# Kernel optimization log

Hardware: AMD Instinct MI355X
Metric: run time of the kernel (lower is better)

## Reference

```python
import jax, jax.numpy as jnp
import numpy as np

S, B, D, H = 2048, 64, 128, 128


def setup_inputs() -> dict:
    key = jax.random.key(0)
    ks = jax.random.split(key, 7)
    scale = 1.0 / np.sqrt(H)
    return {
        "input": jax.random.normal(ks[0], (S, B, D), dtype=jnp.float32),
        "time": jax.random.uniform(ks[1], (S, B, 1), dtype=jnp.float32),
        "W_ih": jax.random.normal(ks[2], (4 * H, D), dtype=jnp.float32) * scale,
        "W_hh": jax.random.normal(ks[3], (4 * H, H), dtype=jnp.float32) * scale,
        "b": jax.random.normal(ks[4], (4 * H,), dtype=jnp.float32) * scale,
        "w_t": jax.random.uniform(ks[5], (H,), dtype=jnp.float32),
        "b_t": jax.random.uniform(ks[6], (H,), dtype=jnp.float32),
    }


def reference(input, time, W_ih, W_hh, b, w_t, b_t):
    # ReverseLSTMLayer: run a time-conditioned LSTM cell over REVERSED time steps,
    # then re-reverse the stacked outputs. state starts at zeros (state=None).
    Bsz = input.shape[1]
    Hd = W_hh.shape[1]

    def step(state, xt):
        x, t = xt  # x: [B, D], t: [B, 1]
        h, c = state
        gates = x @ W_ih.T + h @ W_hh.T + b  # [B, 4H]
        i_, f_, g_, o_ = jnp.split(gates, 4, axis=-1)
        i_ = jax.nn.sigmoid(i_)
        f_ = jax.nn.sigmoid(f_)
        g_ = jnp.tanh(g_)
        o_ = jax.nn.sigmoid(o_)
        # learned exponential time decay on the carried cell state (T-LSTM style)
        decay = jnp.exp(-jax.nn.relu(t * w_t + b_t))  # [B, H]
        c = f_ * c * decay + i_ * g_
        h = o_ * jnp.tanh(c)
        return (h, c), h

    init = (jnp.zeros((Bsz, Hd), input.dtype), jnp.zeros((Bsz, Hd), input.dtype))
    # iterate over reversed sequence, then reverse outputs back
    (h, c), ys_rev = jax.lax.scan(step, init, (input[::-1], time[::-1]))
    outputs = ys_rev[::-1]  # [S, B, H]
    return outputs, (h, c)
```

## Files before the change

### kernel.cpp

```cpp
#include <hip/hip_runtime.h>

#define S_LEN 2048
#define B_SZ  64
#define D_IN  128
#define H_SZ  128
#define G4    512

typedef __attribute__((ext_vector_type(4))) float     floatx4;
typedef __attribute__((ext_vector_type(2))) float     floatx2;
typedef __attribute__((ext_vector_type(8))) _Float16  half8;
typedef __attribute__((ext_vector_type(4))) _Float16  half4;
typedef __attribute__((ext_vector_type(2))) _Float16  half2_t;

template<int CTRL>
__device__ __forceinline__ float qperm(float v) {
  return __int_as_float(
      __builtin_amdgcn_mov_dpp(__float_as_int(v), CTRL, 0xF, 0xF, true));
}

template<int P>
__device__ __forceinline__ half2_t h2ext(half8 v) {
  return __builtin_shufflevector(v, v, 2 * P, 2 * P + 1);
}

__device__ __forceinline__ void lds_barrier() {
  asm volatile("s_waitcnt lgkmcnt(0)\n\ts_barrier" ::: "memory");
}

__global__ __launch_bounds__(256) void gx_gemm(
    const float* __restrict__ X,
    const float* __restrict__ Wih,
    const float* __restrict__ bias,
    _Float16* __restrict__ gx)
{
  __shared__ _Float16 Wl[128][136];
  const int tid  = threadIdx.x;
  const int lane = tid & 63;
  const int wv   = tid >> 6;
  const int b    = blockIdx.y;
  const int T0   = blockIdx.x * 256;
  const int m    = lane & 15;
  const int q    = lane >> 4;

  const float LOG2E = 1.4426950408889634f;

  half8 afrag[4][4];
  #pragma unroll
  for (int rg = 0; rg < 4; ++rg) {
    const int t = T0 + rg * 64 + wv * 16 + m;
    const float* xrow = X + ((size_t)t * B_SZ + b) * D_IN;
    #pragma unroll
    for (int kf = 0; kf < 4; ++kf) {
      const int k0 = kf * 32 + q * 8;
      floatx4 v0 = *(const floatx4*)(xrow + k0);
      floatx4 v1 = *(const floatx4*)(xrow + k0 + 4);
      half8 a;
      a[0] = (_Float16)v0.x; a[1] = (_Float16)v0.y;
      a[2] = (_Float16)v0.z; a[3] = (_Float16)v0.w;
      a[4] = (_Float16)v1.x; a[5] = (_Float16)v1.y;
      a[6] = (_Float16)v1.z; a[7] = (_Float16)v1.w;
      afrag[rg][kf] = a;
    }
  }

  for (int nc = 0; nc < 4; ++nc) {
    const float sc = (nc == 2) ? (-2.0f * LOG2E) : (-LOG2E);
    __syncthreads();
    for (int i = tid; i < 128 * 32; i += 256) {
      const int row = i >> 5;
      const int c4  = (i & 31) * 4;
      floatx4 v = *(const floatx4*)(Wih + ((size_t)nc * 128 + row) * D_IN + c4);
      Wl[row][c4 + 0] = (_Float16)v.x;
      Wl[row][c4 + 1] = (_Float16)v.y;
      Wl[row][c4 + 2] = (_Float16)v.z;
      Wl[row][c4 + 3] = (_Float16)v.w;
    }
    __syncthreads();

    #pragma unroll
    for (int nt = 0; nt < 8; ++nt) {
      const int n0  = nc * 128 + nt * 16;
      const int nlo = nt * 16 + m;
      const float bv = bias[n0 + m];
      half8 bfrag[4];
      #pragma unroll
      for (int kf = 0; kf < 4; ++kf)
        bfrag[kf] = *(const half8*)(&Wl[nlo][kf * 32 + q * 8]);
      #pragma unroll
      for (int rg = 0; rg < 4; ++rg) {
        floatx4 acc = {bv, bv, bv, bv};
        #pragma unroll
        for (int kf = 0; kf < 4; ++kf)
          acc = __builtin_amdgcn_mfma_f32_16x16x32_f16(afrag[rg][kf],
                                                       bfrag[kf], acc, 0, 0, 0);
        const int tbase = T0 + rg * 64 + wv * 16 + q * 4;
        half4 hv;
        hv[0] = (_Float16)(acc[0] * sc);
        hv[1] = (_Float16)(acc[1] * sc);
        hv[2] = (_Float16)(acc[2] * sc);
        hv[3] = (_Float16)(acc[3] * sc);
        *(half4*)(gx + ((size_t)b * G4 + n0 + m) * S_LEN + tbase) = hv;
      }
    }
  }
}

__device__ __forceinline__ float fd(half2_t a, half2_t b, float c) {
  return __builtin_amdgcn_fdot2(a, b, c, false);
}

__device__ __forceinline__ half8 wcvt(const float* __restrict__ p, float sc) {
  floatx4 v0 = *(const floatx4*)p;
  floatx4 v1 = *(const floatx4*)(p + 4);
  half8 h;
  h[0] = (_Float16)(v0.x * sc); h[1] = (_Float16)(v0.y * sc);
  h[2] = (_Float16)(v0.z * sc); h[3] = (_Float16)(v0.w * sc);
  h[4] = (_Float16)(v1.x * sc); h[5] = (_Float16)(v1.y * sc);
  h[6] = (_Float16)(v1.z * sc); h[7] = (_Float16)(v1.w * sc);
  return h;
}

#define PIN_WEIGHTS()                                                         \
  asm volatile(""                                                             \
               : "+v"(w00), "+v"(w01), "+v"(w02), "+v"(w03),                  \
                 "+v"(w10), "+v"(w11), "+v"(w12), "+v"(w13),                  \
                 "+v"(w20), "+v"(w21), "+v"(w22), "+v"(w23),                  \
                 "+v"(w30), "+v"(w31), "+v"(w32), "+v"(w33),                  \
                 "+v"(wt), "+v"(bt))

#define DOT8(HV, WA, WB, WC, WD)                                              \
  {                                                                           \
    q0a = fd(h2ext<0>(HV), h2ext<0>(WA), q0a);                                \
    q1a = fd(h2ext<0>(HV), h2ext<0>(WB), q1a);                                \
    q2a = fd(h2ext<0>(HV), h2ext<0>(WC), q2a);                                \
    q3a = fd(h2ext<0>(HV), h2ext<0>(WD), q3a);                                \
    q0a = fd(h2ext<1>(HV), h2ext<1>(WA), q0a);                                \
    q1a = fd(h2ext<1>(HV), h2ext<1>(WB), q1a);                                \
    q2a = fd(h2ext<1>(HV), h2ext<1>(WC), q2a);                                \
    q3a = fd(h2ext<1>(HV), h2ext<1>(WD), q3a);                                \
    q0b = fd(h2ext<2>(HV), h2ext<2>(WA), q0b);                                \
    q1b = fd(h2ext<2>(HV), h2ext<2>(WB), q1b);                                \
    q2b = fd(h2ext<2>(HV), h2ext<2>(WC), q2b);                                \
    q3b = fd(h2ext<2>(HV), h2ext<2>(WD), q3b);                                \
    q0b = fd(h2ext<3>(HV), h2ext<3>(WA), q0b);                                \
    q1b = fd(h2ext<3>(HV), h2ext<3>(WB), q1b);                                \
    q2b = fd(h2ext<3>(HV), h2ext<3>(WC), q2b);                                \
    q3b = fd(h2ext<3>(HV), h2ext<3>(WD), q3b);                                \
  }

#define GATE(HR, GXV, TMV, CVAR, HVAR)                                        \
  {                                                                           \
    half8 hv0 = *(const half8*)((HR) + 0 * 32 + tt * 8);                      \
    half8 hv1 = *(const half8*)((HR) + 1 * 32 + tt * 8);                      \
    half8 hv2 = *(const half8*)((HR) + 2 * 32 + tt * 8);                      \
    half8 hv3 = *(const half8*)((HR) + 3 * 32 + tt * 8);                      \
    float q0a = 0.f, q0b = 0.f, q1a = 0.f, q1b = 0.f;                         \
    float q2a = 0.f, q2b = 0.f, q3a = 0.f, q3b = 0.f;                         \
    DOT8(hv0, w00, w10, w20, w30);                                            \
    DOT8(hv1, w01, w11, w21, w31);                                            \
    DOT8(hv2, w02, w12, w22, w32);                                            \
    DOT8(hv3, w03, w13, w23, w33);                                            \
    float a0 = q0a + q0b, a1 = q1a + q1b, a2 = q2a + q2b, a3 = q3a + q3b;     \
    a0 += qperm<0xB1>(a0); a1 += qperm<0xB1>(a1);                             \
    a2 += qperm<0xB1>(a2); a3 += qperm<0xB1>(a3);                             \
    a0 += qperm<0x4E>(a0); a1 += qperm<0x4E>(a1);                             \
    a2 += qperm<0x4E>(a2); a3 += qperm<0x4E>(a3);                             \
    float pre = (tt & 1) ? ((tt & 2) ? a3 : a1) : ((tt & 2) ? a2 : a0);       \
    pre += (GXV);            \
    const float e  = __builtin_amdgcn_exp2f(pre);                             \
    const float v  = fmaf(am, __builtin_amdgcn_rcpf(1.0f + e), aa);           \
    float z = fmaf((TMV), wt, bt);                  \
    z = fminf(z, 0.0f);                                   \
    const float d  = __builtin_amdgcn_exp2f(z);                               \
    const float p2 = qperm<0x4E>(v);                                          \
    const float fv = (tt == 1) ? v : p2;                                      \
    const float r  = odd ? fv * (d * (CVAR)) : v * p2;                        \
    const float cn = r + qperm<0xB1>(r);                                      \
    (CVAR) = cn;                                                              \
    const float e2 = __builtin_amdgcn_exp2f(-2.0f * LOG2E * cn);              \
    const float th = fmaf(2.0f, __builtin_amdgcn_rcpf(1.0f + e2), -1.0f);     \
    (HVAR) = v * th;                                                          \
  }

#define SUB(K, TMV, RP, WP)                                                   \
  {                                                                           \
    const float g0 = (float)cur8[K];                                          \
    float h0;                                                                 \
    GATE(&hbuf[RP][0], g0, (TMV), c, h0);                                     \
    if (tt == 3) {                                                            \
      hbuf[WP][col] = (_Float16)h0;                                           \
      const int tcur = blk * 8 + K;                                           \
      out[((size_t)tcur << 13) + bH + col] = h0;                              \
      if (tcur == 0) {                                                        \
        float* hf = out + (size_t)S_LEN * B_SZ * H_SZ;                        \
        hf[bH + col] = h0;                                                    \
        hf[(size_t)B_SZ * H_SZ + bH + col] = c;                               \
      }                                                                       \
    }                                                                         \
    lds_barrier();                                                            \
  }

__global__ __launch_bounds__(512)
__attribute__((amdgpu_waves_per_eu(2, 2)))
void lstm_rev(
    const _Float16* __restrict__ gx,
    const float* __restrict__ timep,
    const float* __restrict__ Whh,
    const float* __restrict__ w_tp,
    const float* __restrict__ b_tp,
    float* __restrict__ out)
{
  __shared__ __align__(16) _Float16 hbuf[2][H_SZ];
  __shared__ __align__(16) float    tml[S_LEN];
  const int tid = threadIdx.x;
  const int b   = blockIdx.x;
  const int tt  = tid & 3;
  const int col = tid >> 2;
  const int j   = tt * 128 + col;

  const float LOG2E = 1.4426950408889634f;

  #pragma unroll
  for (int k = 0; k < 4; ++k) {
    const int idx = tid + k * 512;
    tml[idx] = timep[(idx << 6) + b];
  }

  half8 w00, w01, w02, w03, w10, w11, w12, w13;
  half8 w20, w21, w22, w23, w30, w31, w32, w33;
  {
    const float s1 = -LOG2E, s2 = -2.0f * LOG2E;
    const float* r0 = Whh + (size_t)(0 * 128 + col) * H_SZ + tt * 8;
    const float* r1 = Whh + (size_t)(1 * 128 + col) * H_SZ + tt * 8;
    const float* r2 = Whh + (size_t)(2 * 128 + col) * H_SZ + tt * 8;
    const float* r3 = Whh + (size_t)(3 * 128 + col) * H_SZ + tt * 8;
    w00 = wcvt(r0 +  0, s1); w01 = wcvt(r0 + 32, s1);
    w02 = wcvt(r0 + 64, s1); w03 = wcvt(r0 + 96, s1);
    w10 = wcvt(r1 +  0, s1); w11 = wcvt(r1 + 32, s1);
    w12 = wcvt(r1 + 64, s1); w13 = wcvt(r1 + 96, s1);
    w20 = wcvt(r2 +  0, s2); w21 = wcvt(r2 + 32, s2);
    w22 = wcvt(r2 + 64, s2); w23 = wcvt(r2 + 96, s2);
    w30 = wcvt(r3 +  0, s1); w31 = wcvt(r3 + 32, s1);
    w32 = wcvt(r3 + 64, s1); w33 = wcvt(r3 + 96, s1);
  }

  float wt = -LOG2E * w_tp[col];
  float bt = -LOG2E * b_tp[col];
  const float am  = (tt == 2) ? 2.0f : 1.0f;
  const float aa  = (tt == 2) ? -1.0f : 0.0f;
  const bool  odd = (tt & 1) != 0;

  if (tid < 2 * H_SZ) ((_Float16*)hbuf)[tid] = (_Float16)0.0f;
  __syncthreads();

  const _Float16* gxr = gx + ((size_t)b * G4 + j) * S_LEN;
  const size_t bH = (size_t)b * H_SZ;

  half8 cur8 = *(const half8*)(gxr + 255 * 8);
  half8 nxt8 = *(const half8*)(gxr + 254 * 8);

  float c = 0.0f;

  for (int blk = 255; blk >= 0; --blk) {
    PIN_WEIGHTS();
    const int pfb = (blk >= 2) ? blk - 2 : 0;
    half8 fut8 = *(const half8*)(gxr + pfb * 8);
    const floatx4 tmA = *(const floatx4*)(&tml[blk * 8 + 4]);
    const floatx4 tmB = *(const floatx4*)(&tml[blk * 8 + 0]);

    SUB(7, tmA.w, 0, 1)
    SUB(6, tmA.z, 1, 0)
    SUB(5, tmA.y, 0, 1)
    SUB(4, tmA.x, 1, 0)
    SUB(3, tmB.w, 0, 1)
    SUB(2, tmB.z, 1, 0)
    SUB(1, tmB.y, 0, 1)
    SUB(0, tmB.x, 1, 0)

    cur8 = nxt8;
    nxt8 = fut8;
  }
}

extern "C" void kernel_launch(void* const* d_in, const int* in_sizes, int n_in,
                              void* d_out, int out_size, void* d_ws, size_t ws_size,
                              hipStream_t stream) {
  const float* input = (const float*)d_in[0];
  const float* timep = (const float*)d_in[1];
  const float* W_ih  = (const float*)d_in[2];
  const float* W_hh  = (const float*)d_in[3];
  const float* bias  = (const float*)d_in[4];
  const float* w_t   = (const float*)d_in[5];
  const float* b_t   = (const float*)d_in[6];
  float* out = (float*)d_out;

  _Float16* gx = (_Float16*)d_ws;

  gx_gemm<<<dim3(S_LEN / 256, B_SZ), dim3(256), 0, stream>>>(
      input, W_ih, bias, gx);

  lstm_rev<<<dim3(B_SZ), dim3(512), 0, stream>>>(
      gx, timep, W_hh, w_t, b_t, out);
}
```

Before: 1.287 ms.

## Process two batch elements per block in the recurrent LSTM kernel

Each workgroup now runs two independent batch rows through the sequential recurrence, sharing the register-resident W_hh weights and interleaving the two gate computations between barriers. Half as many blocks are launched, and the per-step barrier and latency cost is spread over twice the work, giving more instruction-level parallelism within each step. The trade-off is lower parallelism across the GPU (32 blocks) and a longer per-step critical path. A dead DOT8 copy containing a typo is defined and then immediately undefined.

```diff
diff --git a/kernel.cpp b/kernel.cpp
--- a/kernel.cpp
+++ b/kernel.cpp
@@ -128,6 +128,27 @@
                  "+v"(w30), "+v"(w31), "+v"(w32), "+v"(w33),                  \
                  "+v"(wt), "+v"(bt))
 
+#define DOT8(HV, WA, WB, WC, WD)                                              \
+  {                                                                           \
+    q0a = fd(h2ext<0>(HV), h2ext<0>(WA), q0a);                                \
+    q1a = fd(h2ext<0>(HV), h2ext<0>(WB), q1a);                                \
+    q2a = fd(h2ext<0>(HV), h2ext<0>(WC), q2a);                                \
+    q3a = fd(h2ext<0>(HV), h2ext<0>(WD), q3a);                                \
+    q0a = fd(h2ext<1>(HV), h2ext<1>(WA), q0a);                                \
+    q1a = fd(h2ext<1>(HV), h2ext<1>(WB), q1a);                                \
+    q2a = fd(h2ext<1>(HV), h2ext<1>(WC), q2a);                                \
+    q3a = fd(h2ext<1>(HV), h2ext<1>(WD), q3a);                                \
+    q0b = fd(h2ext<2>(HV), h2ext<2>(WA), q0b);                                \
+    q1b = fd(h2ext<2>(HV), h2ext<2>(WB), q1b);                                \
+    q2b = fd(h2ext<2>(HV), h2ext<2>(WC), q2b);                                \
+    q3b = fd(h2ext<2>(HV), h2ext<2>(WD), q3b);                                \
+    q0b = fd(h2ext<3>(HV), h2ext<3>(WA), q0b);                                \
+    q1b = fd(h2ext<3>(HV), h2ext<3>(WB), q1b);                                \
+    q2b = fd(h2ext<3>(HV), h2ext<3>(WD), q2b);                                \
+    q3b = fd(h2ext<3>(HV), h2ext<3>(WD), q3b);                                \
+  }
+
+#undef DOT8
 #define DOT8(HV, WA, WB, WC, WD)                                              \
   {                                                                           \
     q0a = fd(h2ext<0>(HV), h2ext<0>(WA), q0a);                                \
@@ -182,19 +203,27 @@
     (HVAR) = v * th;                                                          \
   }
 
-#define SUB(K, TMV, RP, WP)                                                   \
+#define SUB2(K, TM0, TM1, RP, WP)                                             \
   {                                                                           \
-    const float g0 = (float)cur8[K];                                          \
-    float h0;                                                                 \
-    GATE(&hbuf[RP][0], g0, (TMV), c, h0);                                     \
+    const float g0 = (float)cura[K];                                          \
+    const float g1 = (float)curb[K];                                          \
+    float h0, h1;                                                             \
+    GATE(&hbuf[0][RP][0], g0, (TM0), c0, h0);                                 \
+    GATE(&hbuf[1][RP][0], g1, (TM1), c1, h1);                                 \
     if (tt == 3) {                                                            \
-      hbuf[WP][col] = (_Float16)h0;                                           \
+      hbuf[0][WP][col] = (_Float16)h0;                                        \
+      hbuf[1][WP][col] = (_Float16)h1;                                        \
       const int tcur = blk * 8 + K;                                           \
-      out[((size_t)tcur << 13) + bH + col] = h0;                              \
+      float* o = out + ((size_t)tcur << 13) + b0H + col;                      \
+      o[0]    = h0;                                                           \
+      o[H_SZ] = h1;                                                           \
       if (tcur == 0) {                                                        \
         float* hf = out + (size_t)S_LEN * B_SZ * H_SZ;                        \
-        hf[bH + col] = h0;                                                    \
-        hf[(size_t)B_SZ * H_SZ + bH + col] = c;                               \
+        hf[b0H + col]        = h0;                                            \
+        hf[b0H + H_SZ + col] = h1;                                            \
+        float* cf = hf + (size_t)B_SZ * H_SZ;                                 \
+        cf[b0H + col]        = c0;                                            \
+        cf[b0H + H_SZ + col] = c1;                                            \
       }                                                                       \
     }                                                                         \
     lds_barrier();                                                            \
@@ -210,10 +239,10 @@
     const float* __restrict__ b_tp,
     float* __restrict__ out)
 {
-  __shared__ __align__(16) _Float16 hbuf[2][H_SZ];
-  __shared__ __align__(16) float    tml[S_LEN];
+  __shared__ __align__(16) _Float16 hbuf[2][2][H_SZ];
+  __shared__ __align__(16) floatx2  tml[S_LEN];
   const int tid = threadIdx.x;
-  const int b   = blockIdx.x;
+  const int b0  = blockIdx.x * 2;
   const int tt  = tid & 3;
   const int col = tid >> 2;
   const int j   = tt * 128 + col;
@@ -223,7 +252,10 @@
   #pragma unroll
   for (int k = 0; k < 4; ++k) {
     const int idx = tid + k * 512;
-    tml[idx] = timep[(idx << 6) + b];
+    floatx2 tv;
+    tv.x = timep[(idx << 6) + b0];
+    tv.y = timep[(idx << 6) + b0 + 1];
+    tml[idx] = tv;
   }
 
   half8 w00, w01, w02, w03, w10, w11, w12, w13;
@@ -250,35 +282,41 @@
   const float aa  = (tt == 2) ? -1.0f : 0.0f;
   const bool  odd = (tt & 1) != 0;
 
-  if (tid < 2 * H_SZ) ((_Float16*)hbuf)[tid] = (_Float16)0.0f;
+  ((_Float16*)hbuf)[tid] = (_Float16)0.0f;
   __syncthreads();
 
-  const _Float16* gxr = gx + ((size_t)b * G4 + j) * S_LEN;
-  const size_t bH = (size_t)b * H_SZ;
-
-  half8 cur8 = *(const half8*)(gxr + 255 * 8);
-  half8 nxt8 = *(const half8*)(gxr + 254 * 8);
-
-  float c = 0.0f;
+  const _Float16* gxra = gx + ((size_t)b0 * G4 + j) * S_LEN;
+  const _Float16* gxrb = gxra + (size_t)G4 * S_LEN;
+  const size_t b0H = (size_t)b0 * H_SZ;
+
+  half8 cura = *(const half8*)(gxra + 255 * 8);
+  half8 curb = *(const half8*)(gxrb + 255 * 8);
+  half8 nxta = *(const half8*)(gxra + 254 * 8);
+  half8 nxtb = *(const half8*)(gxrb + 254 * 8);
+
+  float c0 = 0.0f, c1 = 0.0f;
 
   for (int blk = 255; blk >= 0; --blk) {
     PIN_WEIGHTS();
     const int pfb = (blk >= 2) ? blk - 2 : 0;
-    half8 fut8 = *(const half8*)(gxr + pfb * 8);
-    const floatx4 tmA = *(const floatx4*)(&tml[blk * 8 + 4]);
-    const floatx4 tmB = *(const floatx4*)(&tml[blk * 8 + 0]);
-
-    SUB(7, tmA.w, 0, 1)
-    SUB(6, tmA.z, 1, 0)
-    SUB(5, tmA.y, 0, 1)
-    SUB(4, tmA.x, 1, 0)
-    SUB(3, tmB.w, 0, 1)
-    SUB(2, tmB.z, 1, 0)
-    SUB(1, tmB.y, 0, 1)
-    SUB(0, tmB.x, 1, 0)
-
-    cur8 = nxt8;
-    nxt8 = fut8;
+    half8 futa = *(const half8*)(gxra + pfb * 8);
+    half8 futb = *(const half8*)(gxrb + pfb * 8);
+    const floatx4 tmQ0 = *(const floatx4*)(&tml[blk * 8 + 0]);
+    const floatx4 tmQ1 = *(const floatx4*)(&tml[blk * 8 + 2]);
+    const floatx4 tmQ2 = *(const floatx4*)(&tml[blk * 8 + 4]);
+    const floatx4 tmQ3 = *(const floatx4*)(&tml[blk * 8 + 6]);
+
+    SUB2(7, tmQ3.z, tmQ3.w, 0, 1)
+    SUB2(6, tmQ3.x, tmQ3.y, 1, 0)
+    SUB2(5, tmQ2.z, tmQ2.w, 0, 1)
+    SUB2(4, tmQ2.x, tmQ2.y, 1, 0)
+    SUB2(3, tmQ1.z, tmQ1.w, 0, 1)
+    SUB2(2, tmQ1.x, tmQ1.y, 1, 0)
+    SUB2(1, tmQ0.z, tmQ0.w, 0, 1)
+    SUB2(0, tmQ0.x, tmQ0.y, 1, 0)
+
+    cura = nxta; nxta = futa;
+    curb = nxtb; nxtb = futb;
   }
 }
 
@@ -299,6 +337,6 @@
   gx_gemm<<<dim3(S_LEN / 256, B_SZ), dim3(256), 0, stream>>>(
       input, W_ih, bias, gx);
 
-  lstm_rev<<<dim3(B_SZ), dim3(512), 0, stream>>>(
+  lstm_rev<<<dim3(B_SZ / 2), dim3(512), 0, stream>>>(
       gx, timep, W_hh, w_t, b_t, out);
 }
```

Result: slower. 2.237 ms (+73.8%).

## Halve LSTM block to 256 threads, each computing two hidden columns

Applied to the files above, without the earlier changes.

The recurrent kernel now launches 256 threads per batch row instead of 512. Each thread holds the W_hh slices for two hidden columns (col and col+64) in registers and computes both gate sets per step, sharing the h vector loads from LDS. The aim is to cut per-step barrier cost across fewer waves (4 instead of 8) and to raise per-thread instruction-level parallelism. In exchange, register use roughly doubles (waves_per_eu set to 1) and the serial work per thread per step doubles, which may lengthen the critical path.

```diff
diff --git a/kernel.cpp b/kernel.cpp
--- a/kernel.cpp
+++ b/kernel.cpp
@@ -120,88 +120,118 @@
   return h;
 }
 
-#define PIN_WEIGHTS()                                                         \
+#define PIN_A()                                                               \
   asm volatile(""                                                             \
-               : "+v"(w00), "+v"(w01), "+v"(w02), "+v"(w03),                  \
-                 "+v"(w10), "+v"(w11), "+v"(w12), "+v"(w13),                  \
-                 "+v"(w20), "+v"(w21), "+v"(w22), "+v"(w23),                  \
-                 "+v"(w30), "+v"(w31), "+v"(w32), "+v"(w33),                  \
-                 "+v"(wt), "+v"(bt))
-
-#define DOT8(HV, WA, WB, WC, WD)                                              \
+               : "+v"(wa00), "+v"(wa01), "+v"(wa02), "+v"(wa03),              \
+                 "+v"(wa10), "+v"(wa11), "+v"(wa12), "+v"(wa13),              \
+                 "+v"(wa20), "+v"(wa21), "+v"(wa22), "+v"(wa23),              \
+                 "+v"(wa30), "+v"(wa31), "+v"(wa32), "+v"(wa33),              \
+                 "+v"(wtA), "+v"(btA))
+#define PIN_B()                                                               \
+  asm volatile(""                                                             \
+               : "+v"(wb00), "+v"(wb01), "+v"(wb02), "+v"(wb03),              \
+                 "+v"(wb10), "+v"(wb11), "+v"(wb12), "+v"(wb13),              \
+                 "+v"(wb20), "+v"(wb21), "+v"(wb22), "+v"(wb23),              \
+                 "+v"(wb30), "+v"(wb31), "+v"(wb32), "+v"(wb33),              \
+                 "+v"(wtB), "+v"(btB))
+
+#define DOT8P(Q, HV, W0, W1, W2, W3)                                          \
   {                                                                           \
-    q0a = fd(h2ext<0>(HV), h2ext<0>(WA), q0a);                                \
-    q1a = fd(h2ext<0>(HV), h2ext<0>(WB), q1a);                                \
-    q2a = fd(h2ext<0>(HV), h2ext<0>(WC), q2a);                                \
-    q3a = fd(h2ext<0>(HV), h2ext<0>(WD), q3a);                                \
-    q0a = fd(h2ext<1>(HV), h2ext<1>(WA), q0a);                                \
-    q1a = fd(h2ext<1>(HV), h2ext<1>(WB), q1a);                                \
-    q2a = fd(h2ext<1>(HV), h2ext<1>(WC), q2a);                                \
-    q3a = fd(h2ext<1>(HV), h2ext<1>(WD), q3a);                                \
-    q0b = fd(h2ext<2>(HV), h2ext<2>(WA), q0b);                                \
-    q1b = fd(h2ext<2>(HV), h2ext<2>(WB), q1b);                                \
-    q2b = fd(h2ext<2>(HV), h2ext<2>(WC), q2b);                                \
-    q3b = fd(h2ext<2>(HV), h2ext<2>(WD), q3b);                                \
-    q0b = fd(h2ext<3>(HV), h2ext<3>(WA), q0b);                                \
-    q1b = fd(h2ext<3>(HV), h2ext<3>(WB), q1b);                                \
-    q2b = fd(h2ext<3>(HV), h2ext<3>(WC), q2b);                                \
-    q3b = fd(h2ext<3>(HV), h2ext<3>(WD), q3b);                                \
-  }
-
-#define GATE(HR, GXV, TMV, CVAR, HVAR)                                        \
+    Q##0a = fd(h2ext<0>(HV), h2ext<0>(W0), Q##0a);                            \
+    Q##1a = fd(h2ext<0>(HV), h2ext<0>(W1), Q##1a);                            \
+    Q##2a = fd(h2ext<0>(HV), h2ext<0>(W2), Q##2a);                            \
+    Q##3a = fd(h2ext<0>(HV), h2ext<0>(W3), Q##3a);                            \
+    Q##0a = fd(h2ext<1>(HV), h2ext<1>(W0), Q##0a);                            \
+    Q##1a = fd(h2ext<1>(HV), h2ext<1>(W1), Q##1a);                            \
+    Q##2a = fd(h2ext<1>(HV), h2ext<1>(W2), Q##2a);                            \
+    Q##3a = fd(h2ext<1>(HV), h2ext<1>(W3), Q##3a);                            \
+    Q##0b = fd(h2ext<2>(HV), h2ext<2>(W0), Q##0b);                            \
+    Q##1b = fd(h2ext<2>(HV), h2ext<2>(W1), Q##1b);                            \
+    Q##2b = fd(h2ext<2>(HV), h2ext<2>(W2), Q##2b);                            \
+    Q##3b = fd(h2ext<2>(HV), h2ext<2>(W3), Q##3b);                            \
+    Q##0b = fd(h2ext<3>(HV), h2ext<3>(W0), Q##0b);                            \
+    Q##1b = fd(h2ext<3>(HV), h2ext<3>(W1), Q##1b);                            \
+    Q##2b = fd(h2ext<3>(HV), h2ext<3>(W2), Q##2b);                            \
+    Q##3b = fd(h2ext<3>(HV), h2ext<3>(W3), Q##3b);                            \
+  }
+
+#define ACT(PRE, TMV, WT, BT, CV, HOUT)                                       \
   {                                                                           \
-    half8 hv0 = *(const half8*)((HR) + 0 * 32 + tt * 8);                      \
-    half8 hv1 = *(const half8*)((HR) + 1 * 32 + tt * 8);                      \
-    half8 hv2 = *(const half8*)((HR) + 2 * 32 + tt * 8);                      \
-    half8 hv3 = *(const half8*)((HR) + 3 * 32 + tt * 8);                      \
-    float q0a = 0.f, q0b = 0.f, q1a = 0.f, q1b = 0.f;                         \
-    float q2a = 0.f, q2b = 0.f, q3a = 0.f, q3b = 0.f;                         \
-    DOT8(hv0, w00, w10, w20, w30);                                            \
-    DOT8(hv1, w01, w11, w21, w31);                                            \
-    DOT8(hv2, w02, w12, w22, w32);                                            \
-    DOT8(hv3, w03, w13, w23, w33);                                            \
-    float a0 = q0a + q0b, a1 = q1a + q1b, a2 = q2a + q2b, a3 = q3a + q3b;     \
-    a0 += qperm<0xB1>(a0); a1 += qperm<0xB1>(a1);                             \
-    a2 += qperm<0xB1>(a2); a3 += qperm<0xB1>(a3);                             \
-    a0 += qperm<0x4E>(a0); a1 += qperm<0x4E>(a1);                             \
-    a2 += qperm<0x4E>(a2); a3 += qperm<0x4E>(a3);                             \
-    float pre = (tt & 1) ? ((tt & 2) ? a3 : a1) : ((tt & 2) ? a2 : a0);       \
-    pre += (GXV);            \
-    const float e  = __builtin_amdgcn_exp2f(pre);                             \
+    const float e  = __builtin_amdgcn_exp2f(PRE);                             \
     const float v  = fmaf(am, __builtin_amdgcn_rcpf(1.0f + e), aa);           \
-    float z = fmaf((TMV), wt, bt);                  \
-    z = fminf(z, 0.0f);                                   \
+    float z = fmaf((TMV), (WT), (BT));                                        \
+    z = fminf(z, 0.0f);                                                       \
     const float d  = __builtin_amdgcn_exp2f(z);                               \
     const float p2 = qperm<0x4E>(v);                                          \
     const float fv = (tt == 1) ? v : p2;                                      \
-    const float r  = odd ? fv * (d * (CVAR)) : v * p2;                        \
+    const float r  = odd ? fv * (d * (CV)) : v * p2;                          \
     const float cn = r + qperm<0xB1>(r);                                      \
-    (CVAR) = cn;                                                              \
+    (CV) = cn;                                                                \
     const float e2 = __builtin_amdgcn_exp2f(-2.0f * LOG2E * cn);              \
     const float th = fmaf(2.0f, __builtin_amdgcn_rcpf(1.0f + e2), -1.0f);     \
-    (HVAR) = v * th;                                                          \
-  }
-
-#define SUB(K, TMV, RP, WP)                                                   \
+    (HOUT) = v * th;                                                          \
+  }
+
+#define SUB2(K, TMV, RP, WP)                                                  \
   {                                                                           \
-    const float g0 = (float)cur8[K];                                          \
-    float h0;                                                                 \
-    GATE(&hbuf[RP][0], g0, (TMV), c, h0);                                     \
+    const float g0 = (float)cur0[K];                                          \
+    const float g1 = (float)cur1[K];                                          \
+    half8 hv0 = *(const half8*)(&hbuf[RP][0] + 0 * 32 + tt * 8);              \
+    half8 hv1 = *(const half8*)(&hbuf[RP][0] + 1 * 32 + tt * 8);              \
+    half8 hv2 = *(const half8*)(&hbuf[RP][0] + 2 * 32 + tt * 8);              \
+    half8 hv3 = *(const half8*)(&hbuf[RP][0] + 3 * 32 + tt * 8);              \
+    float qa0a = 0.f, qa0b = 0.f, qa1a = 0.f, qa1b = 0.f;                     \
+    float qa2a = 0.f, qa2b = 0.f, qa3a = 0.f, qa3b = 0.f;                     \
+    float qb0a = 0.f, qb0b = 0.f, qb1a = 0.f, qb1b = 0.f;                     \
+    float qb2a = 0.f, qb2b = 0.f, qb3a = 0.f, qb3b = 0.f;                     \
+    DOT8P(qa, hv0, wa00, wa10, wa20, wa30);                                   \
+    DOT8P(qb, hv0, wb00, wb10, wb20, wb30);                                   \
+    DOT8P(qa, hv1, wa01, wa11, wa21, wa31);                                   \
+    DOT8P(qb, hv1, wb01, wb11, wb21, wb31);                                   \
+    DOT8P(qa, hv2, wa02, wa12, wa22, wa32);                                   \
+    DOT8P(qb, hv2, wb02, wb12, wb22, wb32);                                   \
+    DOT8P(qa, hv3, wa03, wa13, wa23, wa33);                                   \
+    DOT8P(qb, hv3, wb03, wb13, wb23, wb33);                                   \
+    float aA0 = qa0a + qa0b, aA1 = qa1a + qa1b;                               \
+    float aA2 = qa2a + qa2b, aA3 = qa3a + qa3b;                               \
+    float aB0 = qb0a + qb0b, aB1 = qb1a + qb1b;                               \
+    float aB2 = qb2a + qb2b, aB3 = qb3a + qb3b;                               \
+    aA0 += qperm<0xB1>(aA0); aA1 += qperm<0xB1>(aA1);                         \
+    aA2 += qperm<0xB1>(aA2); aA3 += qperm<0xB1>(aA3);                         \
+    aB0 += qperm<0xB1>(aB0); aB1 += qperm<0xB1>(aB1);                         \
+    aB2 += qperm<0xB1>(aB2); aB3 += qperm<0xB1>(aB3);                         \
+    aA0 += qperm<0x4E>(aA0); aA1 += qperm<0x4E>(aA1);                         \
+    aA2 += qperm<0x4E>(aA2); aA3 += qperm<0x4E>(aA3);                         \
+    aB0 += qperm<0x4E>(aB0); aB1 += qperm<0x4E>(aB1);                         \
+    aB2 += qperm<0x4E>(aB2); aB3 += qperm<0x4E>(aB3);                         \
+    float preA = (tt & 1) ? ((tt & 2) ? aA3 : aA1) : ((tt & 2) ? aA2 : aA0);  \
+    float preB = (tt & 1) ? ((tt & 2) ? aB3 : aB1) : ((tt & 2) ? aB2 : aB0);  \
+    preA += g0;                                                               \
+    preB += g1;                                                               \
+    float hA, hB;                                                             \
+    ACT(preA, (TMV), wtA, btA, cA, hA);                                       \
+    ACT(preB, (TMV), wtB, btB, cB, hB);                                       \
     if (tt == 3) {                                                            \
-      hbuf[WP][col] = (_Float16)h0;                                           \
+      hbuf[WP][col]      = (_Float16)hA;                                      \
+      hbuf[WP][col + 64] = (_Float16)hB;                                      \
       const int tcur = blk * 8 + K;                                           \
-      out[((size_t)tcur << 13) + bH + col] = h0;                              \
+      float* o = out + ((size_t)tcur << 13) + bH + col;                       \
+      o[0]  = hA;                                                             \
+      o[64] = hB;                                                             \
       if (tcur == 0) {                                                        \
         float* hf = out + (size_t)S_LEN * B_SZ * H_SZ;                        \
-        hf[bH + col] = h0;                                                    \
-        hf[(size_t)B_SZ * H_SZ + bH + col] = c;                               \
+        hf[bH + col]      = hA;                                               \
+        hf[bH + col + 64] = hB;                                               \
+        float* cf = hf + (size_t)B_SZ * H_SZ;                                 \
+        cf[bH + col]      = cA;                                               \
+        cf[bH + col + 64] = cB;                                               \
       }                                                                       \
     }                                                                         \
     lds_barrier();                                                            \
   }
 
-__global__ __launch_bounds__(512)
-__attribute__((amdgpu_waves_per_eu(2, 2)))
+__global__ __launch_bounds__(256)
+__attribute__((amdgpu_waves_per_eu(1, 1)))
 void lstm_rev(
     const _Float16* __restrict__ gx,
     const float* __restrict__ timep,
@@ -216,69 +246,91 @@
   const int b   = blockIdx.x;
   const int tt  = tid & 3;
   const int col = tid >> 2;
-  const int j   = tt * 128 + col;
+  const int j0  = tt * 128 + col;
+  const int j1  = j0 + 64;
 
   const float LOG2E = 1.4426950408889634f;
 
   #pragma unroll
-  for (int k = 0; k < 4; ++k) {
-    const int idx = tid + k * 512;
+  for (int k = 0; k < 8; ++k) {
+    const int idx = tid + k * 256;
     tml[idx] = timep[(idx << 6) + b];
   }
 
-  half8 w00, w01, w02, w03, w10, w11, w12, w13;
-  half8 w20, w21, w22, w23, w30, w31, w32, w33;
+  half8 wa00, wa01, wa02, wa03, wa10, wa11, wa12, wa13;
+  half8 wa20, wa21, wa22, wa23, wa30, wa31, wa32, wa33;
+  half8 wb00, wb01, wb02, wb03, wb10, wb11, wb12, wb13;
+  half8 wb20, wb21, wb22, wb23, wb30, wb31, wb32, wb33;
   {
     const float s1 = -LOG2E, s2 = -2.0f * LOG2E;
-    const float* r0 = Whh + (size_t)(0 * 128 + col) * H_SZ + tt * 8;
-    const float* r1 = Whh + (size_t)(1 * 128 + col) * H_SZ + tt * 8;
-    const float* r2 = Whh + (size_t)(2 * 128 + col) * H_SZ + tt * 8;
-    const float* r3 = Whh + (size_t)(3 * 128 + col) * H_SZ + tt * 8;
-    w00 = wcvt(r0 +  0, s1); w01 = wcvt(r0 + 32, s1);
-    w02 = wcvt(r0 + 64, s1); w03 = wcvt(r0 + 96, s1);
-    w10 = wcvt(r1 +  0, s1); w11 = wcvt(r1 + 32, s1);
-    w12 = wcvt(r1 + 64, s1); w13 = wcvt(r1 + 96, s1);
-    w20 = wcvt(r2 +  0, s2); w21 = wcvt(r2 + 32, s2);
-    w22 = wcvt(r2 + 64, s2); w23 = wcvt(r2 + 96, s2);
-    w30 = wcvt(r3 +  0, s1); w31 = wcvt(r3 + 32, s1);
-    w32 = wcvt(r3 + 64, s1); w33 = wcvt(r3 + 96, s1);
-  }
-
-  float wt = -LOG2E * w_tp[col];
-  float bt = -LOG2E * b_tp[col];
+    const float* a0 = Whh + (size_t)(0 * 128 + col) * H_SZ + tt * 8;
+    const float* a1 = Whh + (size_t)(1 * 128 + col) * H_SZ + tt * 8;
+    const float* a2 = Whh + (size_t)(2 * 128 + col) * H_SZ + tt * 8;
+    const float* a3 = Whh + (size_t)(3 * 128 + col) * H_SZ + tt * 8;
+    wa00 = wcvt(a0 +  0, s1); wa01 = wcvt(a0 + 32, s1);
+    wa02 = wcvt(a0 + 64, s1); wa03 = wcvt(a0 + 96, s1);
+    wa10 = wcvt(a1 +  0, s1); wa11 = wcvt(a1 + 32, s1);
+    wa12 = wcvt(a1 + 64, s1); wa13 = wcvt(a1 + 96, s1);
+    wa20 = wcvt(a2 +  0, s2); wa21 = wcvt(a2 + 32, s2);
+    wa22 = wcvt(a2 + 64, s2); wa23 = wcvt(a2 + 96, s2);
+    wa30 = wcvt(a3 +  0, s1); wa31 = wcvt(a3 + 32, s1);
+    wa32 = wcvt(a3 + 64, s1); wa33 = wcvt(a3 + 96, s1);
+    const float* b0p = a0 + (size_t)64 * H_SZ;
+    const float* b1p = a1 + (size_t)64 * H_SZ;
+    const float* b2p = a2 + (size_t)64 * H_SZ;
+    const float* b3p = a3 + (size_t)64 * H_SZ;
+    wb00 = wcvt(b0p +  0, s1); wb01 = wcvt(b0p + 32, s1);
+    wb02 = wcvt(b0p + 64, s1); wb03 = wcvt(b0p + 96, s1);
+    wb10 = wcvt(b1p +  0, s1); wb11 = wcvt(b1p + 32, s1);
+    wb12 = wcvt(b1p + 64, s1); wb13 = wcvt(b1p + 96, s1);
+    wb20 = wcvt(b2p +  0, s2); wb21 = wcvt(b2p + 32, s2);
+    wb22 = wcvt(b2p + 64, s2); wb23 = wcvt(b2p + 96, s2);
+    wb30 = wcvt(b3p +  0, s1); wb31 = wcvt(b3p + 32, s1);
+    wb32 = wcvt(b3p + 64, s1); wb33 = wcvt(b3p + 96, s1);
+  }
+
+  float wtA = -LOG2E * w_tp[col];
+  float btA = -LOG2E * b_tp[col];
+  float wtB = -LOG2E * w_tp[col + 64];
+  float btB = -LOG2E * b_tp[col + 64];
   const float am  = (tt == 2) ? 2.0f : 1.0f;
   const float aa  = (tt == 2) ? -1.0f : 0.0f;
   const bool  odd = (tt & 1) != 0;
 
-  if (tid < 2 * H_SZ) ((_Float16*)hbuf)[tid] = (_Float16)0.0f;
+  ((_Float16*)hbuf)[tid] = (_Float16)0.0f;
   __syncthreads();
 
-  const _Float16* gxr = gx + ((size_t)b * G4 + j) * S_LEN;
+  const _Float16* gxr0 = gx + ((size_t)b * G4 + j0) * S_LEN;
+  const _Float16* gxr1 = gx + ((size_t)b * G4 + j1) * S_LEN;
   const size_t bH = (size_t)b * H_SZ;
 
-  half8 cur8 = *(const half8*)(gxr + 255 * 8);
-  half8 nxt8 = *(const half8*)(gxr + 254 * 8);
-
-  float c = 0.0f;
+  half8 cur0 = *(const half8*)(gxr0 + 255 * 8);
+  half8 cur1 = *(const half8*)(gxr1 + 255 * 8);
+  half8 nxt0 = *(const half8*)(gxr0 + 254 * 8);
+  half8 nxt1 = *(const half8*)(gxr1 + 254 * 8);
+
+  float cA = 0.0f, cB = 0.0f;
 
   for (int blk = 255; blk >= 0; --blk) {
-    PIN_WEIGHTS();
+    PIN_A();
+    PIN_B();
     const int pfb = (blk >= 2) ? blk - 2 : 0;
-    half8 fut8 = *(const half8*)(gxr + pfb * 8);
+    half8 fut0 = *(const half8*)(gxr0 + pfb * 8);
+    half8 fut1 = *(const half8*)(gxr1 + pfb * 8);
     const floatx4 tmA = *(const floatx4*)(&tml[blk * 8 + 4]);
     const floatx4 tmB = *(const floatx4*)(&tml[blk * 8 + 0]);
 
-    SUB(7, tmA.w, 0, 1)
-    SUB(6, tmA.z, 1, 0)
-    SUB(5, tmA.y, 0, 1)
-    SUB(4, tmA.x, 1, 0)
-    SUB(3, tmB.w, 0, 1)
-    SUB(2, tmB.z, 1, 0)
-    SUB(1, tmB.y, 0, 1)
-    SUB(0, tmB.x, 1, 0)
-
-    cur8 = nxt8;
-    nxt8 = fut8;
+    SUB2(7, tmA.w, 0, 1)
+    SUB2(6, tmA.z, 1, 0)
+    SUB2(5, tmA.y, 0, 1)
+    SUB2(4, tmA.x, 1, 0)
+    SUB2(3, tmB.w, 0, 1)
+    SUB2(2, tmB.z, 1, 0)
+    SUB2(1, tmB.y, 0, 1)
+    SUB2(0, tmB.x, 1, 0)
+
+    cur0 = nxt0; nxt0 = fut0;
+    cur1 = nxt1; nxt1 = fut1;
   }
 }
 
@@ -299,6 +351,6 @@
   gx_gemm<<<dim3(S_LEN / 256, B_SZ), dim3(256), 0, stream>>>(
       input, W_ih, bias, gx);
 
-  lstm_rev<<<dim3(B_SZ), dim3(512), 0, stream>>>(
+  lstm_rev<<<dim3(B_SZ), dim3(256), 0, stream>>>(
       gx, timep, W_hh, w_t, b_t, out);
 }
```

Measured after the change: 1.344 ms. 1.04x slower.

## Batch 16 sequences per block and compute recurrent gates with MFMA

Applied to the files above, without the earlier changes.

Replaces the per-batch-row fdot2 recurrence (one block per batch element, 64 blocks) with a block handling 16 batch rows. Each wave computes its 16 hidden units' four gates via 16x16x32 f16 MFMAs against h from LDS, then applies all activations per lane without DPP cross-lane combines. The time values are now read directly from global memory with register prefetch instead of staged in LDS. This launches only 4 blocks, so parallelism across CUs drops sharply. MFMA latency also now sits on the serial per-step critical path.

```diff
diff --git a/kernel.cpp b/kernel.cpp
--- a/kernel.cpp
+++ b/kernel.cpp
@@ -7,24 +7,22 @@
 #define G4    512
 
 typedef __attribute__((ext_vector_type(4))) float     floatx4;
-typedef __attribute__((ext_vector_type(2))) float     floatx2;
 typedef __attribute__((ext_vector_type(8))) _Float16  half8;
 typedef __attribute__((ext_vector_type(4))) _Float16  half4;
-typedef __attribute__((ext_vector_type(2))) _Float16  half2_t;
-
-template<int CTRL>
-__device__ __forceinline__ float qperm(float v) {
-  return __int_as_float(
-      __builtin_amdgcn_mov_dpp(__float_as_int(v), CTRL, 0xF, 0xF, true));
-}
-
-template<int P>
-__device__ __forceinline__ half2_t h2ext(half8 v) {
-  return __builtin_shufflevector(v, v, 2 * P, 2 * P + 1);
-}
 
 __device__ __forceinline__ void lds_barrier() {
   asm volatile("s_waitcnt lgkmcnt(0)\n\ts_barrier" ::: "memory");
+}
+
+__device__ __forceinline__ half8 wcvt(const float* __restrict__ p, float sc) {
+  floatx4 v0 = *(const floatx4*)p;
+  floatx4 v1 = *(const floatx4*)(p + 4);
+  half8 h;
+  h[0] = (_Float16)(v0.x * sc); h[1] = (_Float16)(v0.y * sc);
+  h[2] = (_Float16)(v0.z * sc); h[3] = (_Float16)(v0.w * sc);
+  h[4] = (_Float16)(v1.x * sc); h[5] = (_Float16)(v1.y * sc);
+  h[6] = (_Float16)(v1.z * sc); h[7] = (_Float16)(v1.w * sc);
+  return h;
 }
 
 __global__ __launch_bounds__(256) void gx_gemm(
@@ -105,97 +103,103 @@
   }
 }
 
-__device__ __forceinline__ float fd(half2_t a, half2_t b, float c) {
-  return __builtin_amdgcn_fdot2(a, b, c, false);
-}
-
-__device__ __forceinline__ half8 wcvt(const float* __restrict__ p, float sc) {
-  floatx4 v0 = *(const floatx4*)p;
-  floatx4 v1 = *(const floatx4*)(p + 4);
-  half8 h;
-  h[0] = (_Float16)(v0.x * sc); h[1] = (_Float16)(v0.y * sc);
-  h[2] = (_Float16)(v0.z * sc); h[3] = (_Float16)(v0.w * sc);
-  h[4] = (_Float16)(v1.x * sc); h[5] = (_Float16)(v1.y * sc);
-  h[6] = (_Float16)(v1.z * sc); h[7] = (_Float16)(v1.w * sc);
-  return h;
-}
-
-#define PIN_WEIGHTS()                                                         \
+
+#define PIN_W()                                                               \
   asm volatile(""                                                             \
-               : "+v"(w00), "+v"(w01), "+v"(w02), "+v"(w03),                  \
-                 "+v"(w10), "+v"(w11), "+v"(w12), "+v"(w13),                  \
-                 "+v"(w20), "+v"(w21), "+v"(w22), "+v"(w23),                  \
-                 "+v"(w30), "+v"(w31), "+v"(w32), "+v"(w33),                  \
-                 "+v"(wt), "+v"(bt))
-
-#define DOT8(HV, WA, WB, WC, WD)                                              \
+               : "+v"(wA00), "+v"(wA01), "+v"(wA02), "+v"(wA03),              \
+                 "+v"(wA10), "+v"(wA11), "+v"(wA12), "+v"(wA13),              \
+                 "+v"(wA20), "+v"(wA21), "+v"(wA22), "+v"(wA23),              \
+                 "+v"(wA30), "+v"(wA31), "+v"(wA32), "+v"(wA33))
+
+#define GLOADQ(P, TQ)                                                         \
+  P##00 = *(const half4*)(gxb + (size_t)(0 * 128 + 0) * S_LEN + (TQ));        \
+  P##01 = *(const half4*)(gxb + (size_t)(0 * 128 + 1) * S_LEN + (TQ));        \
+  P##02 = *(const half4*)(gxb + (size_t)(0 * 128 + 2) * S_LEN + (TQ));        \
+  P##03 = *(const half4*)(gxb + (size_t)(0 * 128 + 3) * S_LEN + (TQ));        \
+  P##10 = *(const half4*)(gxb + (size_t)(1 * 128 + 0) * S_LEN + (TQ));        \
+  P##11 = *(const half4*)(gxb + (size_t)(1 * 128 + 1) * S_LEN + (TQ));        \
+  P##12 = *(const half4*)(gxb + (size_t)(1 * 128 + 2) * S_LEN + (TQ));        \
+  P##13 = *(const half4*)(gxb + (size_t)(1 * 128 + 3) * S_LEN + (TQ));        \
+  P##20 = *(const half4*)(gxb + (size_t)(2 * 128 + 0) * S_LEN + (TQ));        \
+  P##21 = *(const half4*)(gxb + (size_t)(2 * 128 + 1) * S_LEN + (TQ));        \
+  P##22 = *(const half4*)(gxb + (size_t)(2 * 128 + 2) * S_LEN + (TQ));        \
+  P##23 = *(const half4*)(gxb + (size_t)(2 * 128 + 3) * S_LEN + (TQ));        \
+  P##30 = *(const half4*)(gxb + (size_t)(3 * 128 + 0) * S_LEN + (TQ));        \
+  P##31 = *(const half4*)(gxb + (size_t)(3 * 128 + 1) * S_LEN + (TQ));        \
+  P##32 = *(const half4*)(gxb + (size_t)(3 * 128 + 2) * S_LEN + (TQ));        \
+  P##33 = *(const half4*)(gxb + (size_t)(3 * 128 + 3) * S_LEN + (TQ));
+
+#define GROT()                                                                \
+  gc00 = gn00; gc01 = gn01; gc02 = gn02; gc03 = gn03;                         \
+  gc10 = gn10; gc11 = gn11; gc12 = gn12; gc13 = gn13;                         \
+  gc20 = gn20; gc21 = gn21; gc22 = gn22; gc23 = gn23;                         \
+  gc30 = gn30; gc31 = gn31; gc32 = gn32; gc33 = gn33;                         \
+  tc0 = tn0; tc1 = tn1; tc2 = tn2; tc3 = tn3;
+
+#define TLOADQ(P, TQ)                                                         \
+  P##0 = tmb[(size_t)((TQ) + 0) * B_SZ];                                      \
+  P##1 = tmb[(size_t)((TQ) + 1) * B_SZ];                                      \
+  P##2 = tmb[(size_t)((TQ) + 2) * B_SZ];                                      \
+  P##3 = tmb[(size_t)((TQ) + 3) * B_SZ];
+
+#define ACT1(PI, PF, PG, PO, TMV, WTR, BTR, CR, HR)                           \
   {                                                                           \
-    q0a = fd(h2ext<0>(HV), h2ext<0>(WA), q0a);                                \
-    q1a = fd(h2ext<0>(HV), h2ext<0>(WB), q1a);                                \
-    q2a = fd(h2ext<0>(HV), h2ext<0>(WC), q2a);                                \
-    q3a = fd(h2ext<0>(HV), h2ext<0>(WD), q3a);                                \
-    q0a = fd(h2ext<1>(HV), h2ext<1>(WA), q0a);                                \
-    q1a = fd(h2ext<1>(HV), h2ext<1>(WB), q1a);                                \
-    q2a = fd(h2ext<1>(HV), h2ext<1>(WC), q2a);                                \
-    q3a = fd(h2ext<1>(HV), h2ext<1>(WD), q3a);                                \
-    q0b = fd(h2ext<2>(HV), h2ext<2>(WA), q0b);                                \
-    q1b = fd(h2ext<2>(HV), h2ext<2>(WB), q1b);                                \
-    q2b = fd(h2ext<2>(HV), h2ext<2>(WC), q2b);                                \
-    q3b = fd(h2ext<2>(HV), h2ext<2>(WD), q3b);                                \
-    q0b = fd(h2ext<3>(HV), h2ext<3>(WA), q0b);                                \
-    q1b = fd(h2ext<3>(HV), h2ext<3>(WB), q1b);                                \
-    q2b = fd(h2ext<3>(HV), h2ext<3>(WC), q2b);                                \
-    q3b = fd(h2ext<3>(HV), h2ext<3>(WD), q3b);                                \
-  }
-
-#define GATE(HR, GXV, TMV, CVAR, HVAR)                                        \
+    const float is = __builtin_amdgcn_rcpf(1.0f + __builtin_amdgcn_exp2f(PI));\
+    const float fs = __builtin_amdgcn_rcpf(1.0f + __builtin_amdgcn_exp2f(PF));\
+    const float gt = fmaf(2.0f,                                               \
+        __builtin_amdgcn_rcpf(1.0f + __builtin_amdgcn_exp2f(PG)), -1.0f);     \
+    const float os = __builtin_amdgcn_rcpf(1.0f + __builtin_amdgcn_exp2f(PO));\
+    const float z  = fminf(fmaf((TMV), (WTR), (BTR)), 0.0f);                  \
+    const float d  = __builtin_amdgcn_exp2f(z);                               \
+    (CR) = fmaf(fs * d, (CR), is * gt);                                       \
+    const float et = __builtin_amdgcn_exp2f(-2.0f * LOG2E * (CR));            \
+    const float th = fmaf(2.0f, __builtin_amdgcn_rcpf(1.0f + et), -1.0f);     \
+    (HR) = os * th;                                                           \
+  }
+
+#define SUBK(K, RP, WP, TMV)                                                  \
   {                                                                           \
-    half8 hv0 = *(const half8*)((HR) + 0 * 32 + tt * 8);                      \
-    half8 hv1 = *(const half8*)((HR) + 1 * 32 + tt * 8);                      \
-    half8 hv2 = *(const half8*)((HR) + 2 * 32 + tt * 8);                      \
-    half8 hv3 = *(const half8*)((HR) + 3 * 32 + tt * 8);                      \
-    float q0a = 0.f, q0b = 0.f, q1a = 0.f, q1b = 0.f;                         \
-    float q2a = 0.f, q2b = 0.f, q3a = 0.f, q3b = 0.f;                         \
-    DOT8(hv0, w00, w10, w20, w30);                                            \
-    DOT8(hv1, w01, w11, w21, w31);                                            \
-    DOT8(hv2, w02, w12, w22, w32);                                            \
-    DOT8(hv3, w03, w13, w23, w33);                                            \
-    float a0 = q0a + q0b, a1 = q1a + q1b, a2 = q2a + q2b, a3 = q3a + q3b;     \
-    a0 += qperm<0xB1>(a0); a1 += qperm<0xB1>(a1);                             \
-    a2 += qperm<0xB1>(a2); a3 += qperm<0xB1>(a3);                             \
-    a0 += qperm<0x4E>(a0); a1 += qperm<0x4E>(a1);                             \
-    a2 += qperm<0x4E>(a2); a3 += qperm<0x4E>(a3);                             \
-    float pre = (tt & 1) ? ((tt & 2) ? a3 : a1) : ((tt & 2) ? a2 : a0);       \
-    pre += (GXV);            \
-    const float e  = __builtin_amdgcn_exp2f(pre);                             \
-    const float v  = fmaf(am, __builtin_amdgcn_rcpf(1.0f + e), aa);           \
-    float z = fmaf((TMV), wt, bt);                  \
-    z = fminf(z, 0.0f);                                   \
-    const float d  = __builtin_amdgcn_exp2f(z);                               \
-    const float p2 = qperm<0x4E>(v);                                          \
-    const float fv = (tt == 1) ? v : p2;                                      \
-    const float r  = odd ? fv * (d * (CVAR)) : v * p2;                        \
-    const float cn = r + qperm<0xB1>(r);                                      \
-    (CVAR) = cn;                                                              \
-    const float e2 = __builtin_amdgcn_exp2f(-2.0f * LOG2E * cn);              \
-    const float th = fmaf(2.0f, __builtin_amdgcn_rcpf(1.0f + e2), -1.0f);     \
-    (HVAR) = v * th;                                                          \
-  }
-
-#define SUB(K, TMV, RP, WP)                                                   \
-  {                                                                           \
-    const float g0 = (float)cur8[K];                                          \
-    float h0;                                                                 \
-    GATE(&hbuf[RP][0], g0, (TMV), c, h0);                                     \
-    if (tt == 3) {                                                            \
-      hbuf[WP][col] = (_Float16)h0;                                           \
-      const int tcur = blk * 8 + K;                                           \
-      out[((size_t)tcur << 13) + bH + col] = h0;                              \
-      if (tcur == 0) {                                                        \
-        float* hf = out + (size_t)S_LEN * B_SZ * H_SZ;                        \
-        hf[bH + col] = h0;                                                    \
-        hf[(size_t)B_SZ * H_SZ + bH + col] = c;                               \
-      }                                                                       \
+    half8 hb0 = *(const half8*)&hl[RP][bq][0 * 32 + q * 8];                   \
+    half8 hb1 = *(const half8*)&hl[RP][bq][1 * 32 + q * 8];                   \
+    half8 hb2 = *(const half8*)&hl[RP][bq][2 * 32 + q * 8];                   \
+    half8 hb3 = *(const half8*)&hl[RP][bq][3 * 32 + q * 8];                   \
+    floatx4 aI = {(float)gc00[K], (float)gc01[K], (float)gc02[K], (float)gc03[K]}; \
+    floatx4 aF = {(float)gc10[K], (float)gc11[K], (float)gc12[K], (float)gc13[K]}; \
+    floatx4 aG = {(float)gc20[K], (float)gc21[K], (float)gc22[K], (float)gc23[K]}; \
+    floatx4 aO = {(float)gc30[K], (float)gc31[K], (float)gc32[K], (float)gc33[K]}; \
+    aI = __builtin_amdgcn_mfma_f32_16x16x32_f16(wA00, hb0, aI, 0, 0, 0);      \
+    aI = __builtin_amdgcn_mfma_f32_16x16x32_f16(wA01, hb1, aI, 0, 0, 0);      \
+    aI = __builtin_amdgcn_mfma_f32_16x16x32_f16(wA02, hb2, aI, 0, 0, 0);      \
+    aI = __builtin_amdgcn_mfma_f32_16x16x32_f16(wA03, hb3, aI, 0, 0, 0);      \
+    aF = __builtin_amdgcn_mfma_f32_16x16x32_f16(wA10, hb0, aF, 0, 0, 0);      \
+    aF = __builtin_amdgcn_mfma_f32_16x16x32_f16(wA11, hb1, aF, 0, 0, 0);      \
+    aF = __builtin_amdgcn_mfma_f32_16x16x32_f16(wA12, hb2, aF, 0, 0, 0);      \
+    aF = __builtin_amdgcn_mfma_f32_16x16x32_f16(wA13, hb3, aF, 0, 0, 0);      \
+    aG = __builtin_amdgcn_mfma_f32_16x16x32_f16(wA20, hb0, aG, 0, 0, 0);      \
+    aG = __builtin_amdgcn_mfma_f32_16x16x32_f16(wA21, hb1, aG, 0, 0, 0);      \
+    aG = __builtin_amdgcn_mfma_f32_16x16x32_f16(wA22, hb2, aG, 0, 0, 0);      \
+    aG = __builtin_amdgcn_mfma_f32_16x16x32_f16(wA23, hb3, aG, 0, 0, 0);      \
+    aO = __builtin_amdgcn_mfma_f32_16x16x32_f16(wA30, hb0, aO, 0, 0, 0);      \
+    aO = __builtin_amdgcn_mfma_f32_16x16x32_f16(wA31, hb1, aO, 0, 0, 0);      \
+    aO = __builtin_amdgcn_mfma_f32_16x16x32_f16(wA32, hb2, aO, 0, 0, 0);      \
+    aO = __builtin_amdgcn_mfma_f32_16x16x32_f16(wA33, hb3, aO, 0, 0, 0);      \
+    float h0, h1, h2, h3;                                                     \
+    ACT1(aI[0], aF[0], aG[0], aO[0], (TMV), wt0, bt0, c0, h0);                \
+    ACT1(aI[1], aF[1], aG[1], aO[1], (TMV), wt1, bt1, c1, h1);                \
+    ACT1(aI[2], aF[2], aG[2], aO[2], (TMV), wt2, bt2, c2, h2);                \
+    ACT1(aI[3], aF[3], aG[3], aO[3], (TMV), wt3, bt3, c3, h3);                \
+    half4 hv;                                                                 \
+    hv[0] = (_Float16)h0; hv[1] = (_Float16)h1;                               \
+    hv[2] = (_Float16)h2; hv[3] = (_Float16)h3;                               \
+    *(half4*)&hl[WP][bq][hc0] = hv;                                           \
+    const int tcur = tq + (K);                                                \
+    floatx4 ov = {h0, h1, h2, h3};                                            \
+    *(floatx4*)(out + ((size_t)tcur << 13) + ((size_t)b << 7) + hc0) = ov;    \
+    if (tcur == 0) {                                                          \
+      float* hf = out + (size_t)S_LEN * B_SZ * H_SZ;                          \
+      *(floatx4*)(hf + ((size_t)b << 7) + hc0) = ov;                          \
+      floatx4 cv = {c0, c1, c2, c3};                                          \
+      *(floatx4*)(hf + (size_t)B_SZ * H_SZ + ((size_t)b << 7) + hc0) = cv;    \
     }                                                                         \
     lds_barrier();                                                            \
   }
@@ -210,75 +214,73 @@
     const float* __restrict__ b_tp,
     float* __restrict__ out)
 {
-  __shared__ __align__(16) _Float16 hbuf[2][H_SZ];
-  __shared__ __align__(16) float    tml[S_LEN];
+  __shared__ __align__(16) _Float16 hl[2][16][136];
   const int tid = threadIdx.x;
-  const int b   = blockIdx.x;
-  const int tt  = tid & 3;
-  const int col = tid >> 2;
-  const int j   = tt * 128 + col;
+  const int w   = tid >> 6;
+  const int l   = tid & 63;
+  const int bq  = l & 15;
+  const int q   = l >> 4;
+  const int B0  = blockIdx.x * 16;
+  const int b   = B0 + bq;
+  const int hc0 = w * 16 + q * 4;
 
   const float LOG2E = 1.4426950408889634f;
 
-  #pragma unroll
-  for (int k = 0; k < 4; ++k) {
-    const int idx = tid + k * 512;
-    tml[idx] = timep[(idx << 6) + b];
-  }
-
-  half8 w00, w01, w02, w03, w10, w11, w12, w13;
-  half8 w20, w21, w22, w23, w30, w31, w32, w33;
+  half8 wA00, wA01, wA02, wA03, wA10, wA11, wA12, wA13;
+  half8 wA20, wA21, wA22, wA23, wA30, wA31, wA32, wA33;
   {
     const float s1 = -LOG2E, s2 = -2.0f * LOG2E;
-    const float* r0 = Whh + (size_t)(0 * 128 + col) * H_SZ + tt * 8;
-    const float* r1 = Whh + (size_t)(1 * 128 + col) * H_SZ + tt * 8;
-    const float* r2 = Whh + (size_t)(2 * 128 + col) * H_SZ + tt * 8;
-    const float* r3 = Whh + (size_t)(3 * 128 + col) * H_SZ + tt * 8;
-    w00 = wcvt(r0 +  0, s1); w01 = wcvt(r0 + 32, s1);
-    w02 = wcvt(r0 + 64, s1); w03 = wcvt(r0 + 96, s1);
-    w10 = wcvt(r1 +  0, s1); w11 = wcvt(r1 + 32, s1);
-    w12 = wcvt(r1 + 64, s1); w13 = wcvt(r1 + 96, s1);
-    w20 = wcvt(r2 +  0, s2); w21 = wcvt(r2 + 32, s2);
-    w22 = wcvt(r2 + 64, s2); w23 = wcvt(r2 + 96, s2);
-    w30 = wcvt(r3 +  0, s1); w31 = wcvt(r3 + 32, s1);
-    w32 = wcvt(r3 + 64, s1); w33 = wcvt(r3 + 96, s1);
-  }
-
-  float wt = -LOG2E * w_tp[col];
-  float bt = -LOG2E * b_tp[col];
-  const float am  = (tt == 2) ? 2.0f : 1.0f;
-  const float aa  = (tt == 2) ? -1.0f : 0.0f;
-  const bool  odd = (tt & 1) != 0;
-
-  if (tid < 2 * H_SZ) ((_Float16*)hbuf)[tid] = (_Float16)0.0f;
+    const float* r0 = Whh + (size_t)(0 * 128 + w * 16 + bq) * H_SZ + q * 8;
+    const float* r1 = Whh + (size_t)(1 * 128 + w * 16 + bq) * H_SZ + q * 8;
+    const float* r2 = Whh + (size_t)(2 * 128 + w * 16 + bq) * H_SZ + q * 8;
+    const float* r3 = Whh + (size_t)(3 * 128 + w * 16 + bq) * H_SZ + q * 8;
+    wA00 = wcvt(r0 +  0, s1); wA01 = wcvt(r0 + 32, s1);
+    wA02 = wcvt(r0 + 64, s1); wA03 = wcvt(r0 + 96, s1);
+    wA10 = wcvt(r1 +  0, s1); wA11 = wcvt(r1 + 32, s1);
+    wA12 = wcvt(r1 + 64, s1); wA13 = wcvt(r1 + 96, s1);
+    wA20 = wcvt(r2 +  0, s2); wA21 = wcvt(r2 + 32, s2);
+    wA22 = wcvt(r2 + 64, s2); wA23 = wcvt(r2 + 96, s2);
+    wA30 = wcvt(r3 +  0, s1); wA31 = wcvt(r3 + 32, s1);
+    wA32 = wcvt(r3 + 64, s1); wA33 = wcvt(r3 + 96, s1);
+  }
+
+  const floatx4 wtv = *(const floatx4*)(w_tp + hc0);
+  const floatx4 btv = *(const floatx4*)(b_tp + hc0);
+  const float wt0 = -LOG2E * wtv[0], wt1 = -LOG2E * wtv[1];
+  const float wt2 = -LOG2E * wtv[2], wt3 = -LOG2E * wtv[3];
+  const float bt0 = -LOG2E * btv[0], bt1 = -LOG2E * btv[1];
+  const float bt2 = -LOG2E * btv[2], bt3 = -LOG2E * btv[3];
+
+  for (int i = tid; i < 2 * 16 * 136; i += 512)
+    ((_Float16*)hl)[i] = (_Float16)0.0f;
   __syncthreads();
 
-  const _Float16* gxr = gx + ((size_t)b * G4 + j) * S_LEN;
-  const size_t bH = (size_t)b * H_SZ;
-
-  half8 cur8 = *(const half8*)(gxr + 255 * 8);
-  half8 nxt8 = *(const half8*)(gxr + 254 * 8);
-
-  float c = 0.0f;
-
-  for (int blk = 255; blk >= 0; --blk) {
-    PIN_WEIGHTS();
-    const int pfb = (blk >= 2) ? blk - 2 : 0;
-    half8 fut8 = *(const half8*)(gxr + pfb * 8);
-    const floatx4 tmA = *(const floatx4*)(&tml[blk * 8 + 4]);
-    const floatx4 tmB = *(const floatx4*)(&tml[blk * 8 + 0]);
-
-    SUB(7, tmA.w, 0, 1)
-    SUB(6, tmA.z, 1, 0)
-    SUB(5, tmA.y, 0, 1)
-    SUB(4, tmA.x, 1, 0)
-    SUB(3, tmB.w, 0, 1)
-    SUB(2, tmB.z, 1, 0)
-    SUB(1, tmB.y, 0, 1)
-    SUB(0, tmB.x, 1, 0)
-
-    cur8 = nxt8;
-    nxt8 = fut8;
+  const _Float16* gxb = gx + ((size_t)b * G4 + w * 16 + q * 4) * S_LEN;
+  const float*    tmb = timep + b;
+
+  float c0 = 0.0f, c1 = 0.0f, c2 = 0.0f, c3 = 0.0f;
+
+  half4 gc00, gc01, gc02, gc03, gc10, gc11, gc12, gc13;
+  half4 gc20, gc21, gc22, gc23, gc30, gc31, gc32, gc33;
+  half4 gn00, gn01, gn02, gn03, gn10, gn11, gn12, gn13;
+  half4 gn20, gn21, gn22, gn23, gn30, gn31, gn32, gn33;
+  float tc0, tc1, tc2, tc3, tn0, tn1, tn2, tn3;
+  GLOADQ(gc, 511 * 4)
+  TLOADQ(tc, 511 * 4)
+  GLOADQ(gn, 510 * 4)
+  TLOADQ(tn, 510 * 4)
+
+  for (int blk = 511; blk >= 0; --blk) {
+    const int tq = blk * 4;
+    PIN_W();
+    SUBK(3, 0, 1, tc3)
+    SUBK(2, 1, 0, tc2)
+    SUBK(1, 0, 1, tc1)
+    SUBK(0, 1, 0, tc0)
+    GROT()
+    const int pfb = (blk >= 2) ? (blk - 2) * 4 : 0;
+    GLOADQ(gn, pfb)
+    TLOADQ(tn, pfb)
   }
 }
 
@@ -299,6 +301,6 @@
   gx_gemm<<<dim3(S_LEN / 256, B_SZ), dim3(256), 0, stream>>>(
       input, W_ih, bias, gx);
 
-  lstm_rev<<<dim3(B_SZ), dim3(512), 0, stream>>>(
+  lstm_rev<<<dim3(B_SZ / 16), dim3(512), 0, stream>>>(
       gx, timep, W_hh, w_t, b_t, out);
 }
```

Result: slower. 3.738 ms (+190.5%).
